# Performance work log

Hardware: AMD Instinct MI355X
Metric: run time of the kernel (lower is better)

Reference implementation:

```python
import jax, jax.numpy as jnp
import numpy as np

B, H, S, Dh = 8, 16, 1028, 64
G = 32
L2 = (2 * G - 1) ** 2  # 3969 relative-position entries
HID = 32
R_VAL = 4  # register-token cutoff


def setup_inputs() -> dict:
    key = jax.random.key(0)
    ks = jax.random.split(key, 7)
    return {
        "q": jax.random.normal(ks[0], (B, H, S, Dh), jnp.float32),
        "k": jax.random.normal(ks[1], (B, H, S, Dh), jnp.float32),
        "v": jax.random.normal(ks[2], (B, H, S, Dh), jnp.float32),
        # normalized log-spaced relative coords in [-1, 1], Swin-v2 style
        "rel_table": jax.random.uniform(ks[3], (L2, 2), jnp.float32, -1.0, 1.0),
        "W1": jax.random.normal(ks[4], (2, HID), jnp.float32) * 0.1,
        "b1": jnp.zeros((HID,), jnp.float32),
        "W2": jax.random.normal(ks[5], (HID, H), jnp.float32) * 0.02,
        "idx_table": jax.random.randint(ks[6], (S, S), 0, L2, jnp.int32),
        "R": R_VAL,
    }


def reference(q, k, v, rel_table, W1, b1, W2, idx_table, R):
    # CPB MLP: Linear(2->hid) + exact GELU + Linear(hid->H, no bias)
    bt = jax.nn.gelu(rel_table @ W1 + b1, approximate=False) @ W2  # [L2, H]
    # gather per-(q,kv) bias, move head axis front -> [H, S, S]
    bias = jnp.transpose(bt[idx_table], (2, 0, 1))
    pos = jnp.arange(S) >= R
    has_bias = pos[:, None] & pos[None, :]  # [S, S]
    scale = Dh ** -0.5
    scores = jnp.einsum('bhqd,bhkd->bhqk', q, k) * scale  # [B,H,S,S]
    scores = scores + jnp.where(has_bias, bias, 0.0)[None]
    p = jax.nn.softmax(scores, axis=-1)
    return jnp.einsum('bhqk,bhkd->bhqd', p, v)
```

## Files before the change

kernel.cpp:

```cpp
#include <hip/hip_runtime.h>
#include <hip/hip_bf16.h>

#define S_LEN 1028
#define DH 64
#define NHEAD 16
#define NBATCH 8
#define L2N 3969
#define HIDN 32
#define KVB 64
#define NKT 17
#define NQT 17
#define TILE_E 4096
#define LOG2E 1.4426950408889634f
#define NKV_TILES (NKT * NBATCH * NHEAD)
#define SPITCH 1040
#define SPLANE ((size_t)S_LEN * SPITCH)

typedef __bf16 bf16x8 __attribute__((ext_vector_type(8)));
typedef __bf16 bf16x4 __attribute__((ext_vector_type(4)));
typedef float f32x4 __attribute__((ext_vector_type(4)));

__device__ __forceinline__ bf16x8 cvt_bf16x8(float4 a, float4 b) {
  bf16x8 r;
  r[0] = (__bf16)a.x; r[1] = (__bf16)a.y; r[2] = (__bf16)a.z; r[3] = (__bf16)a.w;
  r[4] = (__bf16)b.x; r[5] = (__bf16)b.y; r[6] = (__bf16)b.z; r[7] = (__bf16)b.w;
  return r;
}

__device__ __forceinline__ f32x4 mfma16(bf16x8 a, bf16x8 b, f32x4 c) {
  return __builtin_amdgcn_mfma_f32_16x16x32_bf16(a, b, c, 0, 0, 0);
}

__device__ __forceinline__ float exp2_fast(float x) {
#if __has_builtin(__builtin_amdgcn_exp2f)
  return __builtin_amdgcn_exp2f(x);
#else
  return __expf(x * 0.6931471805599453f);
#endif
}

#define GLD16(gsrc, ldst)                                                     \
  __builtin_amdgcn_global_load_lds(                                           \
      (const __attribute__((address_space(1))) void*)(gsrc),                  \
      (__attribute__((address_space(3))) void*)(ldst), 16, 0, 0)

__global__ void cpb_table_lh(const float* __restrict__ rel,
                             const float* __restrict__ W1,
                             const float* __restrict__ b1,
                             const float* __restrict__ W2,
                             float* __restrict__ bt,
                             __bf16* __restrict__ bt16) {
  int i = blockIdx.x * blockDim.x + threadIdx.x;
  if (i >= L2N) return;
  float x = rel[2 * i], y = rel[2 * i + 1];
  float acc[NHEAD];
#pragma unroll
  for (int h = 0; h < NHEAD; ++h) acc[h] = 0.f;
#pragma unroll
  for (int j = 0; j < HIDN; ++j) {
    float t = fmaf(x, W1[j], fmaf(y, W1[HIDN + j], b1[j]));
    float g = 0.5f * t * (1.f + erff(t * 0.70710678118654752f));
#pragma unroll
    for (int h = 0; h < NHEAD; ++h) acc[h] = fmaf(g, W2[j * NHEAD + h], acc[h]);
  }
#pragma unroll
  for (int h = 0; h < NHEAD; ++h) {
    bt[(size_t)i * NHEAD + h] = acc[h];
    bt16[(size_t)i * NHEAD + h] = (__bf16)(acc[h] * LOG2E);
  }
}

__global__ __launch_bounds__(256) void prep_fused3(
    const int* __restrict__ idx, const __bf16* __restrict__ bt16,
    const int* __restrict__ Rp, const float* __restrict__ kg,
    const float* __restrict__ vg, __bf16* __restrict__ bias,
    __bf16* __restrict__ Kb, __bf16* __restrict__ Vb) {
  const int tid = threadIdx.x;
  const int bid = blockIdx.x;
  __shared__ __align__(16) char smem[64 * 68 * 4];

  int kvid = -1, bias_id = -1;
  if (bid < 4112) {
    if ((bid & 1) == 0) bias_id = bid >> 1;
    else kvid = bid >> 1;
  } else {
    kvid = 2056 + (bid - 4112);
  }

  if (bias_id >= 0) {
    const int qrow = bias_id >> 1, half = bias_id & 1;
    const int base = half * 512;
    __bf16(*strip)[520] = (__bf16(*)[520])smem;
    const int R = Rp[0];
    const bool qok = (qrow >= R);
    bf16x8 z8;
#pragma unroll
    for (int j = 0; j < 8; ++j) z8[j] = (__bf16)0.f;

    const int ka = base + tid, kb2 = base + 256 + tid;
    const int la = idx[(size_t)qrow * S_LEN + ka];
    const int lb = idx[(size_t)qrow * S_LEN + kb2];
    bf16x8 va0 = *(const bf16x8*)(bt16 + (size_t)la * 16);
    bf16x8 va1 = *(const bf16x8*)(bt16 + (size_t)la * 16 + 8);
    bf16x8 vb0 = *(const bf16x8*)(bt16 + (size_t)lb * 16);
    bf16x8 vb1 = *(const bf16x8*)(bt16 + (size_t)lb * 16 + 8);
    const bool ona = qok && (ka >= R);
    const bool onb = qok && (kb2 >= R);
    if (!ona) { va0 = z8; va1 = z8; }
    if (!onb) { vb0 = z8; vb1 = z8; }
#pragma unroll
    for (int h = 0; h < 8; ++h) {
      strip[h][tid] = va0[h];
      strip[h][256 + tid] = vb0[h];
      strip[8 + h][tid] = va1[h];
      strip[8 + h][256 + tid] = vb1[h];
    }
    __syncthreads();
    {
      const int h = tid >> 4, seg = tid & 15;
      __bf16* dst = bias + (size_t)h * SPLANE + (size_t)qrow * SPITCH + base + seg * 32;
#pragma unroll
      for (int j = 0; j < 4; ++j)
        *(bf16x8*)(dst + j * 8) = *(bf16x8*)&strip[h][seg * 32 + j * 8];
    }
    if (half && tid < 64) {
      const int kt = tid & 3, h = tid >> 2;
      const int k = 1024 + kt;
      const int l = idx[(size_t)qrow * S_LEN + k];
      const bool on = qok && (k >= R);
      bias[(size_t)h * SPLANE + (size_t)qrow * SPITCH + k] =
          on ? bt16[(size_t)l * 16 + h] : (__bf16)0.f;
    }
  } else {
    if (kvid >= NKV_TILES) return;
    const int it = kvid % NKT, bh = kvid / NKT;
    const int kb = it * KVB;
    const float* kp = kg + (size_t)bh * S_LEN * DH;
    const float* vp = vg + (size_t)bh * S_LEN * DH;
    __bf16* kout = Kb + ((size_t)bh * NKT + it) * TILE_E;
    __bf16* vout = Vb + ((size_t)bh * NKT + it) * TILE_E;

    for (int i = tid; i < 512; i += 256) {
      const int rho = i >> 3, gx = i & 7;
      const int e = ((rho & 15) << 2) | (rho >> 4);
      const int key = kb + e;
      const int gsrc = gx ^ (rho & 7);
      float4 a = {0.f, 0.f, 0.f, 0.f}, b = {0.f, 0.f, 0.f, 0.f};
      if (key < S_LEN) {
        a = *(const float4*)(kp + (size_t)key * DH + gsrc * 8);
        b = *(const float4*)(kp + (size_t)key * DH + gsrc * 8 + 4);
      }
      *(bf16x8*)(kout + (size_t)rho * 64 + gx * 8) = cvt_bf16x8(a, b);
    }

    float(*vt)[68] = (float(*)[68])smem;
    for (int i = tid; i < 1024; i += 256) {
      const int row = i >> 4, c4 = i & 15;
      const int key = kb + row;
      float4 a = {0.f, 0.f, 0.f, 0.f};
      if (key < S_LEN) a = *(const float4*)(vp + (size_t)key * DH + c4 * 4);
      *(float4*)&vt[row][c4 * 4] = a;
    }
    __syncthreads();
    for (int i = tid; i < 512; i += 256) {
      const int d = i >> 3, gx = i & 7;
      const int kg8 = (gx ^ (d & 7)) * 8;
      bf16x8 o;
#pragma unroll
      for (int j = 0; j < 8; ++j) o[j] = (__bf16)vt[kg8 + j][d];
      *(bf16x8*)(vout + (size_t)d * 64 + gx * 8) = o;
    }
  }
}

#define TILE_STEP(ITC, MASKED) do {                                           \
    const int buf_ = (ITC) & 1;                                               \
    const int kk_ = (ITC) * KVB + 4 * m;                                      \
    bf16x4 bias4_[4];                                                         \
    _Pragma("unroll")                                                         \
    for (int r = 0; r < 4; ++r) {                                             \
      bf16x4 z_; z_[0] = (__bf16)0.f; z_[1] = (__bf16)0.f;                    \
      z_[2] = (__bf16)0.f; z_[3] = (__bf16)0.f;                               \
      bias4_[r] = (!(MASKED) || kk_ < S_LEN)                                  \
                      ? *(const bf16x4*)(brow[r] + kk_) : z_;                 \
    }                                                                         \
    __builtin_amdgcn_s_barrier();                                             \
    {                                                                         \
      const int nit_ = ((ITC) + 1 < NKT) ? (ITC) + 1 : 0;                     \
      const __bf16* gk_ = KbT + (size_t)nit_ * TILE_E + wave * 1024 + lo16;   \
      const __bf16* gv_ = VbT + (size_t)nit_ * TILE_E + wave * 1024 + lo16;   \
      __bf16* lk_ = &Kt[buf_ ^ 1][0][0] + wave * 1024;                        \
      __bf16* lv_ = &Vt[buf_ ^ 1][0][0] + wave * 1024;                        \
      GLD16(gk_, lk_); GLD16(gk_ + 512, lk_ + 512);                           \
      GLD16(gv_, lv_); GLD16(gv_ + 512, lv_ + 512);                           \
    }                                                                         \
    asm volatile("s_waitcnt vmcnt(8)" ::: "memory");                          \
    __builtin_amdgcn_s_barrier();                                             \
    __builtin_amdgcn_sched_barrier(0x7);   \
    f32x4 sc_[4];                                                             \
    __builtin_amdgcn_s_setprio(1);                                            \
    _Pragma("unroll")                                                         \
    for (int c = 0; c < 4; ++c) {                                             \
      f32x4 a_;                                                               \
      _Pragma("unroll")                                                       \
      for (int r = 0; r < 4; ++r) a_[r] = (float)bias4_[r][c];                \
      _Pragma("unroll")                                                       \
      for (int dc = 0; dc < 2; ++dc) {                                        \
        bf16x8 kf_ = *(bf16x8*)&Kt[buf_][c * 16 + m][(dc * 32 + g * 8) ^ sw_m]; \
        a_ = mfma16(qf[dc], kf_, a_);                                         \
      }                                                                       \
      sc_[c] = a_;                                                            \
    }                                                                         \
    __builtin_amdgcn_s_setprio(0);                                            \
    _Pragma("unroll")                                                         \
    for (int r = 0; r < 4; ++r) {                                             \
      float p0_ = exp2_fast(sc_[0][r]);                                       \
      float p1_ = exp2_fast(sc_[1][r]);                                       \
      float p2_ = exp2_fast(sc_[2][r]);                                       \
      float p3_ = exp2_fast(sc_[3][r]);                                       \
      if (MASKED) {                                                           \
        const float kvf_ = (kk_ < S_LEN) ? 1.f : 0.f;                         \
        lsum[r] += kvf_ * ((p0_ + p1_) + (p2_ + p3_));                        \
      } else {                                                                \
        lsum[r] += (p0_ + p1_) + (p2_ + p3_);                                 \
      }                                                                       \
      bf16x4 pb_;                                                             \
      pb_[0] = (__bf16)p0_; pb_[1] = (__bf16)p1_;                             \
      pb_[2] = (__bf16)p2_; pb_[3] = (__bf16)p3_;                             \
      const int row_ = g * 4 + r;                                             \
      *(bf16x4*)&Pl[wave][row_][(4 * m) ^ ((row_ & 7) << 3)] = pb_;           \
    }                                                                         \
    __builtin_amdgcn_s_setprio(1);                                            \
    _Pragma("unroll")                                                         \
    for (int kc = 0; kc < 2; ++kc) {                                          \
      bf16x8 pf_ = *(bf16x8*)&Pl[wave][m][(kc * 32 + g * 8) ^ sw_m];          \
      _Pragma("unroll")                                                       \
      for (int t = 0; t < 4; ++t) {                                           \
        bf16x8 vf_ = *(bf16x8*)&Vt[buf_][t * 16 + m][(kc * 32 + g * 8) ^ sw_m]; \
        acc_o[t] = mfma16(pf_, vf_, acc_o[t]);                                \
      }                                                                       \
    }                                                                         \
    __builtin_amdgcn_s_setprio(0);                                            \
  } while (0)

__global__ __launch_bounds__(256, 4) void flex_attn_v4x(
    const float* __restrict__ qg, const __bf16* __restrict__ Kb,
    const __bf16* __restrict__ Vb, const __bf16* __restrict__ biasG,
    float* __restrict__ out) {
  const int h = blockIdx.x;
  const int y = blockIdx.y;
  const int qt = y % NQT;
  const int b = y / NQT;
  const int bh = b * NHEAD + h;
  const int tid = threadIdx.x;
  const int wave = tid >> 6, lane = tid & 63;
  const int g = lane >> 4, m = lane & 15;

  __shared__ __align__(16) __bf16 Kt[2][KVB][64];
  __shared__ __align__(16) __bf16 Vt[2][DH][64];
  __shared__ __align__(16) __bf16 Pl[4][16][64];

  const __bf16* KbT = Kb + (size_t)bh * NKT * TILE_E;
  const __bf16* VbT = Vb + (size_t)bh * NKT * TILE_E;
  const __bf16* bp = biasG + (size_t)h * SPLANE;
  const float* qp = qg + (size_t)bh * S_LEN * DH;

  const int qrow = qt * 64 + wave * 16 + m;
  const float qs = 0.125f * LOG2E;
  bf16x8 qf[2];
#pragma unroll
  for (int dc = 0; dc < 2; ++dc) {
    float4 a = {0.f, 0.f, 0.f, 0.f}, bb = {0.f, 0.f, 0.f, 0.f};
    if (qrow < S_LEN) {
      a = *(const float4*)(qp + (size_t)qrow * DH + dc * 32 + g * 8);
      bb = *(const float4*)(qp + (size_t)qrow * DH + dc * 32 + g * 8 + 4);
    }
    a.x *= qs; a.y *= qs; a.z *= qs; a.w *= qs;
    bb.x *= qs; bb.y *= qs; bb.z *= qs; bb.w *= qs;
    qf[dc] = cvt_bf16x8(a, bb);
  }

  const int qb4 = qt * 64 + wave * 16 + g * 4;
  const __bf16* brow[4];
#pragma unroll
  for (int r = 0; r < 4; ++r) {
    int qq = qb4 + r; if (qq > S_LEN - 1) qq = S_LEN - 1;
    brow[r] = bp + (size_t)qq * SPITCH;
  }

  f32x4 acc_o[4];
#pragma unroll
  for (int t = 0; t < 4; ++t) acc_o[t] = (f32x4){0.f, 0.f, 0.f, 0.f};
  float lsum[4] = {0.f, 0.f, 0.f, 0.f};

  const int sw_m = (m & 7) << 3;
  const int lo16 = lane * 8;

  {
    const __bf16* gk = KbT + wave * 1024 + lo16;
    const __bf16* gv = VbT + wave * 1024 + lo16;
    __bf16* lk = &Kt[0][0][0] + wave * 1024;
    __bf16* lv = &Vt[0][0][0] + wave * 1024;
    GLD16(gk, lk); GLD16(gk + 512, lk + 512);
    GLD16(gv, lv); GLD16(gv + 512, lv + 512);
  }

#pragma unroll 2
  for (int it = 0; it < 16; ++it) {
    TILE_STEP(it, false);
  }
  TILE_STEP(16, true);

#pragma unroll
  for (int r = 0; r < 4; ++r) {
    float s = lsum[r];
    s += __shfl_xor(s, 1);
    s += __shfl_xor(s, 2);
    s += __shfl_xor(s, 4);
    s += __shfl_xor(s, 8);
    const int qq = qb4 + r;
    if (qq >= S_LEN) continue;
    const float inv = 1.f / s;
    float* op = out + (((size_t)bh) * S_LEN + qq) * DH;
#pragma unroll
    for (int t = 0; t < 4; ++t) op[t * 16 + m] = acc_o[t][r] * inv;
  }
}

__global__ __launch_bounds__(256) void bias_expand2(const int* __restrict__ idx,
                                                    const float* __restrict__ bt,
                                                    const int* __restrict__ Rp,
                                                    __bf16* __restrict__ bias) {
  const int qrow = blockIdx.x;
  const int R = Rp[0];
  const bool qok = (qrow >= R);
  const int tid = threadIdx.x;
  __shared__ __align__(16) __bf16 strip[NHEAD][264];
  for (int k0 = 0; k0 < 1024; k0 += 256) {
    const int k = k0 + tid;
    const int l = idx[(size_t)qrow * S_LEN + k];
    const bool on = qok && (k >= R);
    const float4* btv = (const float4*)bt + (size_t)l * 4;
    float va[16];
    *(float4*)&va[0] = btv[0];
    *(float4*)&va[4] = btv[1];
    *(float4*)&va[8] = btv[2];
    *(float4*)&va[12] = btv[3];
#pragma unroll
    for (int h = 0; h < NHEAD; ++h)
      strip[h][tid] = on ? (__bf16)(va[h] * LOG2E) : (__bf16)0.f;
    __syncthreads();
    {
      const int h = tid >> 4, kg2 = tid & 15;
      bf16x8 w0 = *(bf16x8*)&strip[h][kg2 * 16];
      bf16x8 w1 = *(bf16x8*)&strip[h][kg2 * 16 + 8];
      __bf16* dst = bias + (size_t)h * S_LEN * S_LEN + (size_t)qrow * S_LEN + k0 + kg2 * 16;
      *(bf16x8*)dst = w0;
      *(bf16x8*)(dst + 8) = w1;
    }
    __syncthreads();
  }
  if (tid < 64) {
    const int kt = tid & 3, h = tid >> 2;
    const int k = 1024 + kt;
    const int l = idx[(size_t)qrow * S_LEN + k];
    const bool on = qok && (k >= R);
    const float v = bt[(size_t)l * NHEAD + h];
    bias[(size_t)h * S_LEN * S_LEN + (size_t)qrow * S_LEN + k] =
        on ? (__bf16)(v * LOG2E) : (__bf16)0.f;
  }
}

__global__ __launch_bounds__(256, 4) void flex_attn_fast(
    const float* __restrict__ qg, const float* __restrict__ kg,
    const float* __restrict__ vg, const __bf16* __restrict__ biasG,
    float* __restrict__ out) {
  const int b = blockIdx.z, h = blockIdx.y, qt = blockIdx.x;
  const int tid = threadIdx.x;
  const int wave = tid >> 6, lane = tid & 63;
  const int g = lane >> 4, m = lane & 15;

  __shared__ __align__(16) __bf16 Kt[KVB][72];
  __shared__ __align__(16) __bf16 Vt[DH][72];
  __shared__ __align__(16) __bf16 Pl[4][16][72];

  const size_t base = ((size_t)(b * NHEAD + h)) * S_LEN * DH;
  const float* qp = qg + base;
  const float* kp = kg + base;
  const float* vp = vg + base;
  const __bf16* bp = biasG + (size_t)h * S_LEN * S_LEN;

  const int qrow = qt * 64 + wave * 16 + m;
  const float qs = 0.125f * LOG2E;
  bf16x8 qf[2];
#pragma unroll
  for (int dc = 0; dc < 2; ++dc) {
    float4 a = {0.f, 0.f, 0.f, 0.f}, bb = {0.f, 0.f, 0.f, 0.f};
    if (qrow < S_LEN) {
      a = *(const float4*)(qp + (size_t)qrow * DH + dc * 32 + g * 8);
      bb = *(const float4*)(qp + (size_t)qrow * DH + dc * 32 + g * 8 + 4);
    }
    a.x *= qs; a.y *= qs; a.z *= qs; a.w *= qs;
    bb.x *= qs; bb.y *= qs; bb.z *= qs; bb.w *= qs;
    qf[dc] = cvt_bf16x8(a, bb);
  }

  f32x4 acc_o[4];
#pragma unroll
  for (int t = 0; t < 4; ++t) acc_o[t] = (f32x4){0.f, 0.f, 0.f, 0.f};
  float mrow[4], lrow[4];
#pragma unroll
  for (int r = 0; r < 4; ++r) { mrow[r] = -1e30f; lrow[r] = 0.f; }

  const int qb4 = qt * 64 + wave * 16 + g * 4;
  const int eK = wave * 16 + (lane >> 2);
  const int rowK = ((eK & 3) << 4) | (eK >> 2);
  const int colK = (lane & 3) * 16;

  for (int it = 0; it < NKT; ++it) {
    const int kb = it * KVB;
    __syncthreads();
    {
      const int krow = kb + eK;
      float4 a0 = {0,0,0,0}, a1 = {0,0,0,0}, a2 = {0,0,0,0}, a3 = {0,0,0,0};
      if (krow < S_LEN) {
        const float* src = kp + (size_t)krow * DH + colK;
        a0 = *(const float4*)(src);
        a1 = *(const float4*)(src + 4);
        a2 = *(const float4*)(src + 8);
        a3 = *(const float4*)(src + 12);
      }
      *(bf16x8*)&Kt[rowK][colK] = cvt_bf16x8(a0, a1);
      *(bf16x8*)&Kt[rowK][colK + 8] = cvt_bf16x8(a2, a3);
    }
    {
      bf16x8 p0, p1;
#pragma unroll
      for (int t = 0; t < 8; ++t) {
        const int kr = kb + wave * 16 + t;
        p0[t] = (kr < S_LEN) ? (__bf16)vp[(size_t)kr * DH + lane] : (__bf16)0.f;
      }
#pragma unroll
      for (int t = 0; t < 8; ++t) {
        const int kr = kb + wave * 16 + 8 + t;
        p1[t] = (kr < S_LEN) ? (__bf16)vp[(size_t)kr * DH + lane] : (__bf16)0.f;
      }
      *(bf16x8*)&Vt[lane][wave * 16] = p0;
      *(bf16x8*)&Vt[lane][wave * 16 + 8] = p1;
    }

    const int kk = kb + 4 * m;
    const bool kvalid = (kk < S_LEN);
    bf16x4 bias4[4];
#pragma unroll
    for (int r = 0; r < 4; ++r) {
      const int qq = (qb4 + r < S_LEN) ? qb4 + r : S_LEN - 1;
      bf16x4 z; z[0] = (__bf16)0.f; z[1] = (__bf16)0.f; z[2] = (__bf16)0.f; z[3] = (__bf16)0.f;
      bias4[r] = kvalid ? *(const bf16x4*)(bp + (size_t)qq * S_LEN + kk) : z;
    }

    __syncthreads();

    f32x4 sc[4];
#pragma unroll
    for (int c = 0; c < 4; ++c) {
      f32x4 a = (f32x4){0.f, 0.f, 0.f, 0.f};
#pragma unroll
      for (int dc = 0; dc < 2; ++dc) {
        bf16x8 kf = *(bf16x8*)&Kt[c * 16 + m][dc * 32 + g * 8];
        a = mfma16(qf[dc], kf, a);
      }
      sc[c] = a;
    }

#pragma unroll
    for (int r = 0; r < 4; ++r) {
      float s[4];
#pragma unroll
      for (int c = 0; c < 4; ++c)
        s[c] = kvalid ? sc[c][r] + (float)bias4[r][c] : -1e30f;
      float mx = fmaxf(fmaxf(s[0], s[1]), fmaxf(s[2], s[3]));
      mx = fmaxf(mx, __shfl_xor(mx, 1));
      mx = fmaxf(mx, __shfl_xor(mx, 2));
      mx = fmaxf(mx, __shfl_xor(mx, 4));
      mx = fmaxf(mx, __shfl_xor(mx, 8));
      const float mnew = fmaxf(mrow[r], mx);
      const float alpha = exp2_fast(mrow[r] - mnew);
      float p0 = exp2_fast(s[0] - mnew), p1 = exp2_fast(s[1] - mnew);
      float p2 = exp2_fast(s[2] - mnew), p3 = exp2_fast(s[3] - mnew);
      float sum = (p0 + p1) + (p2 + p3);
      sum += __shfl_xor(sum, 1);
      sum += __shfl_xor(sum, 2);
      sum += __shfl_xor(sum, 4);
      sum += __shfl_xor(sum, 8);
      lrow[r] = lrow[r] * alpha + sum;
      mrow[r] = mnew;
      bf16x4 pb;
      pb[0] = (__bf16)p0; pb[1] = (__bf16)p1; pb[2] = (__bf16)p2; pb[3] = (__bf16)p3;
      *(bf16x4*)&Pl[wave][g * 4 + r][4 * m] = pb;
#pragma unroll
      for (int t = 0; t < 4; ++t) acc_o[t][r] *= alpha;
    }

#pragma unroll
    for (int kc = 0; kc < 2; ++kc) {
      bf16x8 pf = *(bf16x8*)&Pl[wave][m][kc * 32 + g * 8];
#pragma unroll
      for (int t = 0; t < 4; ++t) {
        bf16x8 vf = *(bf16x8*)&Vt[t * 16 + m][kc * 32 + g * 8];
        acc_o[t] = mfma16(pf, vf, acc_o[t]);
      }
    }
  }

#pragma unroll
  for (int r = 0; r < 4; ++r) {
    const int qq = qb4 + r;
    if (qq >= S_LEN) continue;
    const float inv = 1.f / lrow[r];
    float* op = out + (((size_t)(b * NHEAD + h)) * S_LEN + qq) * DH;
#pragma unroll
    for (int t = 0; t < 4; ++t) op[t * 16 + m] = acc_o[t][r] * inv;
  }
}

extern "C" void kernel_launch(void* const* d_in, const int* in_sizes, int n_in,
                              void* d_out, int out_size, void* d_ws, size_t ws_size,
                              hipStream_t stream) {
  const float* q = (const float*)d_in[0];
  const float* k = (const float*)d_in[1];
  const float* v = (const float*)d_in[2];
  const float* rel = (const float*)d_in[3];
  const float* W1 = (const float*)d_in[4];
  const float* b1 = (const float*)d_in[5];
  const float* W2 = (const float*)d_in[6];
  const int* idx = (const int*)d_in[7];
  const int* Rp = (const int*)d_in[8];
  float* out = (float*)d_out;

  const size_t bt_bytes = 1u << 18;
  const size_t bt16_bytes = 1u << 17;
  const size_t bias_bytes = (size_t)NHEAD * SPLANE * 2;
  const size_t kv_bytes = (size_t)NBATCH * NHEAD * NKT * TILE_E * 2;

  float* bt = (float*)d_ws;
  __bf16* bt16 = (__bf16*)((char*)d_ws + bt_bytes);
  __bf16* bias = (__bf16*)((char*)d_ws + bt_bytes + bt16_bytes);
  __bf16* Kb = (__bf16*)((char*)d_ws + bt_bytes + bt16_bytes + bias_bytes);
  __bf16* Vb = (__bf16*)((char*)d_ws + bt_bytes + bt16_bytes + bias_bytes + kv_bytes);

  if (ws_size >= bt_bytes + bt16_bytes + bias_bytes + 2 * kv_bytes) {
    cpb_table_lh<<<dim3((L2N + 255) / 256), dim3(256), 0, stream>>>(rel, W1, b1, W2, bt, bt16);
    prep_fused3<<<dim3(4232), dim3(256), 0, stream>>>(idx, bt16, Rp, k, v, bias, Kb, Vb);
    flex_attn_v4x<<<dim3(NHEAD, NQT * NBATCH, 1), dim3(256), 0, stream>>>(q, Kb, Vb, bias, out);
  } else {
    __bf16* bias_f = (__bf16*)((char*)d_ws + bt_bytes + bt16_bytes);
    cpb_table_lh<<<dim3((L2N + 255) / 256), dim3(256), 0, stream>>>(rel, W1, b1, W2, bt, bt16);
    bias_expand2<<<dim3(S_LEN), dim3(256), 0, stream>>>(idx, bt, Rp, bias_f);
    flex_attn_fast<<<dim3(NQT, NHEAD, NBATCH), dim3(256), 0, stream>>>(q, k, v, bias_f, out);
  }
}
```

Before: 247.1 us.

## Prefetch next tile's bias a step ahead and split bias expansion finer

The attention kernel now double-buffers the per-tile bias registers. It loads the next tile's bias right after the QK MMA, so that global load overlaps with softmax and PV instead of sitting at the start of each step. The vmcnt wait is tightened to account for the changed number of outstanding loads. The prep kernel splits each bias row into four 256-wide chunks instead of two, giving more, smaller blocks interleaved with the K/V tiles. Together these add register pressure and rely on correct manual vmcnt counting.

```diff
diff --git a/kernel.cpp b/kernel.cpp
--- a/kernel.cpp
+++ b/kernel.cpp
@@ -70,7 +70,7 @@
   }
 }
 
-__global__ __launch_bounds__(256) void prep_fused3(
+__global__ __launch_bounds__(256) void prep_fused4(
     const int* __restrict__ idx, const __bf16* __restrict__ bt16,
     const int* __restrict__ Rp, const float* __restrict__ kg,
     const float* __restrict__ vg, __bf16* __restrict__ bias,
@@ -80,56 +80,48 @@
   __shared__ __align__(16) char smem[64 * 68 * 4];
 
   int kvid = -1, bias_id = -1;
-  if (bid < 4112) {
-    if ((bid & 1) == 0) bias_id = bid >> 1;
-    else kvid = bid >> 1;
+  if (bid < 6168) {
+    const int grp = bid / 3, rem = bid - 3 * grp;
+    if (rem == 2) kvid = grp;
+    else bias_id = 2 * grp + rem;
   } else {
-    kvid = 2056 + (bid - 4112);
+    kvid = 2056 + (bid - 6168);
   }
 
   if (bias_id >= 0) {
-    const int qrow = bias_id >> 1, half = bias_id & 1;
-    const int base = half * 512;
-    __bf16(*strip)[520] = (__bf16(*)[520])smem;
+    const int qrow = bias_id >> 2, q4 = bias_id & 3;
+    const int base = q4 * 256;
+    __bf16(*strip)[272] = (__bf16(*)[272])smem;
     const int R = Rp[0];
     const bool qok = (qrow >= R);
-    bf16x8 z8;
-#pragma unroll
-    for (int j = 0; j < 8; ++j) z8[j] = (__bf16)0.f;
-
-    const int ka = base + tid, kb2 = base + 256 + tid;
-    const int la = idx[(size_t)qrow * S_LEN + ka];
-    const int lb = idx[(size_t)qrow * S_LEN + kb2];
-    bf16x8 va0 = *(const bf16x8*)(bt16 + (size_t)la * 16);
-    bf16x8 va1 = *(const bf16x8*)(bt16 + (size_t)la * 16 + 8);
-    bf16x8 vb0 = *(const bf16x8*)(bt16 + (size_t)lb * 16);
-    bf16x8 vb1 = *(const bf16x8*)(bt16 + (size_t)lb * 16 + 8);
-    const bool ona = qok && (ka >= R);
-    const bool onb = qok && (kb2 >= R);
-    if (!ona) { va0 = z8; va1 = z8; }
-    if (!onb) { vb0 = z8; vb1 = z8; }
+
+    const int k = base + tid;
+    const int l = idx[(size_t)qrow * S_LEN + k];
+    bf16x8 v0 = *(const bf16x8*)(bt16 + (size_t)l * 16);
+    bf16x8 v1 = *(const bf16x8*)(bt16 + (size_t)l * 16 + 8);
+    if (!(qok && (k >= R))) {
+#pragma unroll
+      for (int j = 0; j < 8; ++j) { v0[j] = (__bf16)0.f; v1[j] = (__bf16)0.f; }
+    }
 #pragma unroll
     for (int h = 0; h < 8; ++h) {
-      strip[h][tid] = va0[h];
-      strip[h][256 + tid] = vb0[h];
-      strip[8 + h][tid] = va1[h];
-      strip[8 + h][256 + tid] = vb1[h];
+      strip[h][tid] = v0[h];
+      strip[8 + h][tid] = v1[h];
     }
     __syncthreads();
     {
       const int h = tid >> 4, seg = tid & 15;
-      __bf16* dst = bias + (size_t)h * SPLANE + (size_t)qrow * SPITCH + base + seg * 32;
-#pragma unroll
-      for (int j = 0; j < 4; ++j)
-        *(bf16x8*)(dst + j * 8) = *(bf16x8*)&strip[h][seg * 32 + j * 8];
-    }
-    if (half && tid < 64) {
+      __bf16* dst = bias + (size_t)h * SPLANE + (size_t)qrow * SPITCH + base + seg * 16;
+      *(bf16x8*)dst = *(bf16x8*)&strip[h][seg * 16];
+      *(bf16x8*)(dst + 8) = *(bf16x8*)&strip[h][seg * 16 + 8];
+    }
+    if (q4 == 3 && tid < 64) {
       const int kt = tid & 3, h = tid >> 2;
-      const int k = 1024 + kt;
-      const int l = idx[(size_t)qrow * S_LEN + k];
-      const bool on = qok && (k >= R);
-      bias[(size_t)h * SPLANE + (size_t)qrow * SPITCH + k] =
-          on ? bt16[(size_t)l * 16 + h] : (__bf16)0.f;
+      const int kk = 1024 + kt;
+      const int lt = idx[(size_t)qrow * S_LEN + kk];
+      const bool on = qok && (kk >= R);
+      bias[(size_t)h * SPLANE + (size_t)qrow * SPITCH + kk] =
+          on ? bt16[(size_t)lt * 16 + h] : (__bf16)0.f;
     }
   } else {
     if (kvid >= NKV_TILES) return;
@@ -173,17 +165,23 @@
   }
 }
 
-#define TILE_STEP(ITC, MASKED) do {                                           \
-    const int buf_ = (ITC) & 1;                                               \
-    const int kk_ = (ITC) * KVB + 4 * m;                                      \
-    bf16x4 bias4_[4];                                                         \
+#define LOADB(BB, ITC) do {                                                   \
+    const int kkL = (ITC) * KVB + 4 * m;                                      \
+    const int kkC = kkL > 1024 ? 1024 : kkL;          \
+    const bool okL = (kkL < S_LEN);                                           \
     _Pragma("unroll")                                                         \
     for (int r = 0; r < 4; ++r) {                                             \
-      bf16x4 z_; z_[0] = (__bf16)0.f; z_[1] = (__bf16)0.f;                    \
-      z_[2] = (__bf16)0.f; z_[3] = (__bf16)0.f;                               \
-      bias4_[r] = (!(MASKED) || kk_ < S_LEN)                                  \
-                      ? *(const bf16x4*)(brow[r] + kk_) : z_;                 \
+      bf16x4 t_ = *(const bf16x4*)(brow[r] + kkC);                            \
+      if (!okL) {                                                             \
+        t_[0] = (__bf16)0.f; t_[1] = (__bf16)0.f;                             \
+        t_[2] = (__bf16)0.f; t_[3] = (__bf16)0.f;                             \
+      }                                                                       \
+      BB[r] = t_;                                                             \
     }                                                                         \
+  } while (0)
+
+#define STEP(ITC, BCUR, BNXT, LOADNEXT, MASKED) do {                          \
+    const int buf_ = (ITC) & 1;                                               \
     __builtin_amdgcn_s_barrier();                                             \
     {                                                                         \
       const int nit_ = ((ITC) + 1 < NKT) ? (ITC) + 1 : 0;                     \
@@ -194,7 +192,7 @@
       GLD16(gk_, lk_); GLD16(gk_ + 512, lk_ + 512);                           \
       GLD16(gv_, lv_); GLD16(gv_ + 512, lv_ + 512);                           \
     }                                                                         \
-    asm volatile("s_waitcnt vmcnt(8)" ::: "memory");                          \
+    asm volatile("s_waitcnt vmcnt(4)" ::: "memory");                          \
     __builtin_amdgcn_s_barrier();                                             \
     __builtin_amdgcn_sched_barrier(0x7);   \
     f32x4 sc_[4];                                                             \
@@ -203,7 +201,7 @@
     for (int c = 0; c < 4; ++c) {                                             \
       f32x4 a_;                                                               \
       _Pragma("unroll")                                                       \
-      for (int r = 0; r < 4; ++r) a_[r] = (float)bias4_[r][c];                \
+      for (int r = 0; r < 4; ++r) a_[r] = (float)BCUR[r][c];                  \
       _Pragma("unroll")                                                       \
       for (int dc = 0; dc < 2; ++dc) {                                        \
         bf16x8 kf_ = *(bf16x8*)&Kt[buf_][c * 16 + m][(dc * 32 + g * 8) ^ sw_m]; \
@@ -212,6 +210,7 @@
       sc_[c] = a_;                                                            \
     }                                                                         \
     __builtin_amdgcn_s_setprio(0);                                            \
+    if (LOADNEXT) LOADB(BNXT, (ITC) + 1);                                     \
     _Pragma("unroll")                                                         \
     for (int r = 0; r < 4; ++r) {                                             \
       float p0_ = exp2_fast(sc_[0][r]);                                       \
@@ -219,7 +218,7 @@
       float p2_ = exp2_fast(sc_[2][r]);                                       \
       float p3_ = exp2_fast(sc_[3][r]);                                       \
       if (MASKED) {                                                           \
-        const float kvf_ = (kk_ < S_LEN) ? 1.f : 0.f;                         \
+        const float kvf_ = (((ITC) * KVB + 4 * m) < S_LEN) ? 1.f : 0.f;       \
         lsum[r] += kvf_ * ((p0_ + p1_) + (p2_ + p3_));                        \
       } else {                                                                \
         lsum[r] += (p0_ + p1_) + (p2_ + p3_);                                 \
@@ -243,7 +242,7 @@
     __builtin_amdgcn_s_setprio(0);                                            \
   } while (0)
 
-__global__ __launch_bounds__(256, 4) void flex_attn_v4x(
+__global__ __launch_bounds__(256, 4) void flex_attn_v6(
     const float* __restrict__ qg, const __bf16* __restrict__ Kb,
     const __bf16* __restrict__ Vb, const __bf16* __restrict__ biasG,
     float* __restrict__ out) {
@@ -296,6 +295,9 @@
   const int sw_m = (m & 7) << 3;
   const int lo16 = lane * 8;
 
+  bf16x4 biasA[4], biasB[4];
+
+  LOADB(biasA, 0);
   {
     const __bf16* gk = KbT + wave * 1024 + lo16;
     const __bf16* gv = VbT + wave * 1024 + lo16;
@@ -305,11 +307,11 @@
     GLD16(gv, lv); GLD16(gv + 512, lv + 512);
   }
 
-#pragma unroll 2
-  for (int it = 0; it < 16; ++it) {
-    TILE_STEP(it, false);
-  }
-  TILE_STEP(16, true);
+  for (int it = 0; it < 16; it += 2) {
+    STEP(it, biasA, biasB, true, false);
+    STEP(it + 1, biasB, biasA, true, false);
+  }
+  STEP(16, biasA, biasB, false, true);
 
 #pragma unroll
   for (int r = 0; r < 4; ++r) {
@@ -551,8 +553,8 @@
 
   if (ws_size >= bt_bytes + bt16_bytes + bias_bytes + 2 * kv_bytes) {
     cpb_table_lh<<<dim3((L2N + 255) / 256), dim3(256), 0, stream>>>(rel, W1, b1, W2, bt, bt16);
-    prep_fused3<<<dim3(4232), dim3(256), 0, stream>>>(idx, bt16, Rp, k, v, bias, Kb, Vb);
-    flex_attn_v4x<<<dim3(NHEAD, NQT * NBATCH, 1), dim3(256), 0, stream>>>(q, Kb, Vb, bias, out);
+    prep_fused4<<<dim3(6288), dim3(256), 0, stream>>>(idx, bt16, Rp, k, v, bias, Kb, Vb);
+    flex_attn_v6<<<dim3(NHEAD, NQT * NBATCH, 1), dim3(256), 0, stream>>>(q, Kb, Vb, bias, out);
   } else {
     __bf16* bias_f = (__bf16*)((char*)d_ws + bt_bytes + bt16_bytes);
     cpb_table_lh<<<dim3((L2N + 255) / 256), dim3(256), 0, stream>>>(rel, W1, b1, W2, bt, bt16);
```

Measured after the change: 253.4 us. +2.5%, slower.
